# Kernel optimization log

Measured on AMD Instinct MI355X. Metric: run time of the kernel, lower is better.

The kernel has to match this reference:

```python
import jax, jax.numpy as jnp
import numpy as np

N_E = 4096
E_DIM = 512
BETA = 0.25


def setup_inputs() -> dict:
    key = jax.random.key(0)
    k1, k2 = jax.random.split(key)
    z = jax.random.normal(k1, (32, 512, E_DIM), dtype=jnp.float32)
    # embedding.weight ~ U(-1/n_e, 1/n_e)
    emb = jax.random.uniform(k2, (N_E, E_DIM), dtype=jnp.float32,
                             minval=-1.0 / N_E, maxval=1.0 / N_E)
    return {"z": z, "emb": emb}


def reference(z, emb):
    B, S, D = z.shape
    zf = z.reshape(-1, D)  # (N, D)
    # squared L2 distances: ||z||^2 + ||e||^2 - 2 z @ e^T  -> (N, n_e)
    d = (jnp.sum(zf * zf, axis=1, keepdims=True)
         + jnp.sum(emb * emb, axis=1)
         - 2.0 * jnp.matmul(zf, emb.T))
    idx = jnp.argmin(d, axis=1)  # (N,)
    z_q = emb[idx].reshape(z.shape)

    # commitment / codebook loss (detach = stop_gradient)
    loss = (jnp.mean((z_q - jax.lax.stop_gradient(z)) ** 2)
            + BETA * jnp.mean((jax.lax.stop_gradient(z_q) - z) ** 2))

    # straight-through estimator
    z_q_st = z + jax.lax.stop_gradient(z_q - z)

    # perplexity via codeword usage histogram (equiv. to mean of one-hots)
    N = zf.shape[0]
    counts = jnp.zeros((N_E,), dtype=z.dtype).at[idx].add(1.0)
    e_mean = counts / N
    perplexity = jnp.exp(-jnp.sum(e_mean * jnp.log(e_mean + 1e-10)))

    return (loss, z_q_st, idx, perplexity)
```

## Files before the change

### kernel.cpp

```cpp
#include <hip/hip_runtime.h>
#include <math.h>

#define NROWS 16384
#define DDIM  512
#define NE    4096
#define NZ    (NROWS * DDIM)
#define MAXC  64
#define MARGIN 2e-3f

typedef __attribute__((ext_vector_type(8))) short bf16x8;
typedef __attribute__((ext_vector_type(4))) float f32x4;

__device__ __forceinline__ float sqr_rn(float x) { return __fmul_rn(x, x); }
__device__ __forceinline__ ushort f2bf(float f) {
    const unsigned u = __float_as_uint(f);
    return (ushort)((u + 0x7fffu + ((u >> 16) & 1u)) >> 16);
}
__device__ __forceinline__ unsigned pack2(float a, float b) {
    return (unsigned)f2bf(a) | ((unsigned)f2bf(b) << 16);
}

__global__ void k_prep(const float* __restrict__ z, const float* __restrict__ emb,
                       ushort* __restrict__ zh, ushort* __restrict__ eh,
                       float* __restrict__ znorm, float* __restrict__ bnorm,
                       unsigned* __restrict__ counts) {
    if (blockIdx.x < 1024) {
        const int lane = threadIdx.x & 63;
        const int c = (int)((blockIdx.x * 256 + threadIdx.x) >> 6);
        const float4* p = (const float4*)(emb + (size_t)c * DDIM);
        const float4 v0 = p[lane * 2], v1 = p[lane * 2 + 1];
        uint4 w; w.x = pack2(v0.x, v0.y); w.y = pack2(v0.z, v0.w);
        w.z = pack2(v1.x, v1.y); w.w = pack2(v1.z, v1.w);
        *(uint4*)(eh + (size_t)c * DDIM + lane * 8) = w;
        float s = v0.x*v0.x + v0.y*v0.y + v0.z*v0.z + v0.w*v0.w
                + v1.x*v1.x + v1.y*v1.y + v1.z*v1.z + v1.w*v1.w;
        #pragma unroll
        for (int m = 32; m; m >>= 1) s += __shfl_xor(s, m);
        if (lane == 0) { bnorm[c] = s; counts[c] = 0u; }
    } else {
        const int t = (int)((blockIdx.x - 1024) * 256 + threadIdx.x);
        const int row = t >> 2, blk = t & 3;
        const float4* p = (const float4*)(z + (size_t)row * DDIM + blk * 128);
        ushort* zo = zh + (size_t)row * DDIM + blk * 128;
        float4 v0 = p[0], v1 = p[1];
        {
            uint4 w; w.x = pack2(v0.x, v0.y); w.y = pack2(v0.z, v0.w);
            w.z = pack2(v1.x, v1.y); w.w = pack2(v1.z, v1.w);
            *(uint4*)zo = w;
        }
        float r[8];
        r[0] = sqr_rn(v0.x); r[1] = sqr_rn(v0.y); r[2] = sqr_rn(v0.z); r[3] = sqr_rn(v0.w);
        r[4] = sqr_rn(v1.x); r[5] = sqr_rn(v1.y); r[6] = sqr_rn(v1.z); r[7] = sqr_rn(v1.w);
        #pragma unroll
        for (int i = 1; i < 16; ++i) {
            v0 = p[2 * i]; v1 = p[2 * i + 1];
            uint4 w; w.x = pack2(v0.x, v0.y); w.y = pack2(v0.z, v0.w);
            w.z = pack2(v1.x, v1.y); w.w = pack2(v1.z, v1.w);
            *(uint4*)(zo + i * 8) = w;
            r[0] = __fadd_rn(r[0], sqr_rn(v0.x)); r[1] = __fadd_rn(r[1], sqr_rn(v0.y));
            r[2] = __fadd_rn(r[2], sqr_rn(v0.z)); r[3] = __fadd_rn(r[3], sqr_rn(v0.w));
            r[4] = __fadd_rn(r[4], sqr_rn(v1.x)); r[5] = __fadd_rn(r[5], sqr_rn(v1.y));
            r[6] = __fadd_rn(r[6], sqr_rn(v1.z)); r[7] = __fadd_rn(r[7], sqr_rn(v1.w));
        }
        const float B = __fadd_rn(__fadd_rn(__fadd_rn(r[0], r[1]), __fadd_rn(r[2], r[3])),
                                  __fadd_rn(__fadd_rn(r[4], r[5]), __fadd_rn(r[6], r[7])));
        const float s01 = __fadd_rn(B, __shfl_xor(B, 1));
        const float zn  = __fadd_rn(s01, __shfl_xor(s01, 2));
        if (blk == 0) znorm[row] = zn;
    }
}

__global__ __launch_bounds__(256) void k_mfma(const ushort* __restrict__ zh,
                                              const ushort* __restrict__ eh,
                                              const float* __restrict__ bnorm,
                                              ushort* __restrict__ sbuf,
                                              float* __restrict__ rowblkmin) {
    __shared__ ushort Af[2][8 * 512];
    __shared__ ushort Bf[2][8 * 512];
    const int tid = threadIdx.x;
    const int lane = tid & 63;
    const int w = tid >> 6;
    const int wrow = (w >> 1) * 64, wcol = (w & 1) * 64;
    const int rbase = blockIdx.x * 128, cbase = blockIdx.y * 128;
    const int sr = tid >> 1, sh = tid & 1;
    const int g  = sr >> 4, r15 = sr & 15;
    const int r16 = lane & 15, g4 = (lane >> 4) * 4;
    const int soff = g * 512 + r15 * 8 + sh * 4;

    const ushort* ga = zh + (size_t)(rbase + sr) * DDIM + sh * 16;
    const ushort* gb = eh + (size_t)(cbase + sr) * DDIM + sh * 16;

    f32x4 acc[4][4];
    #pragma unroll
    for (int i = 0; i < 4; ++i)
        #pragma unroll
        for (int j = 0; j < 4; ++j) acc[i][j] = (f32x4){0.f, 0.f, 0.f, 0.f};

    {
        const uint4 qa0 = *(const uint4*)ga;
        const uint4 qa1 = *(const uint4*)(ga + 8);
        const uint4 qb0 = *(const uint4*)gb;
        const uint4 qb1 = *(const uint4*)(gb + 8);
        ushort* pa = &Af[0][soff];
        *(uint2*)(pa +   0) = make_uint2(qa0.x, qa0.y);
        *(uint2*)(pa + 128) = make_uint2(qa0.z, qa0.w);
        *(uint2*)(pa + 256) = make_uint2(qa1.x, qa1.y);
        *(uint2*)(pa + 384) = make_uint2(qa1.z, qa1.w);
        ushort* pb = &Bf[0][soff];
        *(uint2*)(pb +   0) = make_uint2(qb0.x, qb0.y);
        *(uint2*)(pb + 128) = make_uint2(qb0.z, qb0.w);
        *(uint2*)(pb + 256) = make_uint2(qb1.x, qb1.y);
        *(uint2*)(pb + 384) = make_uint2(qb1.z, qb1.w);
    }
    __syncthreads();

    for (int kb = 0; kb < DDIM; kb += 32) {
        const int cur = (kb >> 5) & 1;
        const bool more = (kb + 32 < DDIM);
        uint4 na0, na1, nb0, nb1;
        if (more) {
            na0 = *(const uint4*)(ga + kb + 32);
            na1 = *(const uint4*)(ga + kb + 40);
            nb0 = *(const uint4*)(gb + kb + 32);
            nb1 = *(const uint4*)(gb + kb + 40);
        }
        bf16x8 af[4], bf[4];
        #pragma unroll
        for (int f = 0; f < 4; ++f) {
            af[f] = *(const bf16x8*)&Af[cur][((wrow >> 4) + f) * 512 + lane * 8];
            bf[f] = *(const bf16x8*)&Bf[cur][((wcol >> 4) + f) * 512 + lane * 8];
        }
        #pragma unroll
        for (int fi = 0; fi < 4; ++fi)
            #pragma unroll
            for (int fj = 0; fj < 4; ++fj)
                acc[fi][fj] = __builtin_amdgcn_mfma_f32_16x16x32_bf16(
                    af[fi], bf[fj], acc[fi][fj], 0, 0, 0);
        if (more) {
            ushort* pa = &Af[cur ^ 1][soff];
            *(uint2*)(pa +   0) = make_uint2(na0.x, na0.y);
            *(uint2*)(pa + 128) = make_uint2(na0.z, na0.w);
            *(uint2*)(pa + 256) = make_uint2(na1.x, na1.y);
            *(uint2*)(pa + 384) = make_uint2(na1.z, na1.w);
            ushort* pb = &Bf[cur ^ 1][soff];
            *(uint2*)(pb +   0) = make_uint2(nb0.x, nb0.y);
            *(uint2*)(pb + 128) = make_uint2(nb0.z, nb0.w);
            *(uint2*)(pb + 256) = make_uint2(nb1.x, nb1.y);
            *(uint2*)(pb + 384) = make_uint2(nb1.z, nb1.w);
            __syncthreads();
        }
    }

    float bn[4];
    #pragma unroll
    for (int fj = 0; fj < 4; ++fj) bn[fj] = bnorm[cbase + wcol + fj * 16 + r16];

    #pragma unroll
    for (int fi = 0; fi < 4; ++fi) {
        #pragma unroll
        for (int r = 0; r < 4; ++r) {
            const int row = rbase + wrow + fi * 16 + g4 + r;
            float s[4];
            #pragma unroll
            for (int fj = 0; fj < 4; ++fj) s[fj] = fmaf(-2.f, acc[fi][fj][r], bn[fj]);
            uint2* sp = (uint2*)(sbuf + (size_t)row * NE + cbase + wcol);
            sp[r16] = make_uint2(pack2(s[0], s[1]), pack2(s[2], s[3]));
            float m = fminf(fminf(s[0], s[1]), fminf(s[2], s[3]));
            #pragma unroll
            for (int x = 1; x < 16; x <<= 1) m = fminf(m, __shfl_xor(m, x));
            if (r16 == 0)
                rowblkmin[(size_t)row * 64 + blockIdx.y * 2 + (w & 1)] = m;
        }
    }
}

__device__ __forceinline__ unsigned long long exact_key(const float4* __restrict__ zp4,
                                                        const float* __restrict__ emb,
                                                        const float* __restrict__ bnorm,
                                                        float zn, int c) {
    const float4* ep4 = (const float4*)(emb + (size_t)c * DDIM);
    float acc = 0.f;
    #pragma unroll 8
    for (int q = 0; q < DDIM / 4; ++q) {
        const float4 zv = zp4[q];
        const float4 ev = ep4[q];
        acc = fmaf(zv.x, ev.x, acc);
        acc = fmaf(zv.y, ev.y, acc);
        acc = fmaf(zv.z, ev.z, acc);
        acc = fmaf(zv.w, ev.w, acc);
    }
    const float s = __fsub_rn(__fadd_rn(zn, bnorm[c]), __fmul_rn(2.f, acc));
    return ((unsigned long long)__float_as_uint(s) << 32) | (unsigned)c;
}

__global__ void k_pg(const ushort* __restrict__ sbuf, const float* __restrict__ rowblkmin,
                     const float* __restrict__ z, const float* __restrict__ emb,
                     const float* __restrict__ znorm, const float* __restrict__ bnorm,
                     float* __restrict__ out, unsigned* __restrict__ counts,
                     float* __restrict__ d2buf) {
    __shared__ int candL[4][MAXC];
    __shared__ unsigned cntL[4];
    const int lane = threadIdx.x & 63;
    const int w = threadIdx.x >> 6;
    const int row = blockIdx.x * 4 + w;
    if (threadIdx.x < 4) cntL[threadIdx.x] = 0u;
    __syncthreads();

    const float bm = rowblkmin[(size_t)row * 64 + lane];
    float gmin = bm;
    #pragma unroll
    for (int m = 32; m; m >>= 1) gmin = fminf(gmin, __shfl_xor(gmin, m));
    const float thr = gmin + MARGIN;
    unsigned long long bmask = __ballot(bm <= thr);
    while (bmask) {
        const int b = __builtin_ctzll(bmask); bmask &= bmask - 1;
        const float val = __uint_as_float(
            (unsigned)sbuf[(size_t)row * NE + b * 64 + lane] << 16);
        if (val <= thr) {
            const unsigned slot = atomicAdd(&cntL[w], 1u);
            if (slot < MAXC)
                candL[w][slot] = b * 64 + (lane & 3) * 16 + (lane >> 2);
        }
    }
    __syncthreads();

    const int cnt = (int)cntL[w];
    int id;
    if (cnt == 1) {
        id = candL[w][0] & (NE - 1);
    } else {
        const float zn = znorm[row];
        const float4* zp4 = (const float4*)(z + (size_t)row * DDIM);
        unsigned long long best = ~0ULL;
        if (cnt >= 2 && cnt <= MAXC) {
            if (lane < cnt)
                best = exact_key(zp4, emb, bnorm, zn, candL[w][lane] & (NE - 1));
        } else {
            for (int c = lane; c < NE; c += 64) {
                const unsigned long long k = exact_key(zp4, emb, bnorm, zn, c);
                if (k < best) best = k;
            }
        }
        #pragma unroll
        for (int m = 32; m; m >>= 1) {
            const unsigned long long ov = __shfl_xor(best, m);
            if (ov < best) best = ov;
        }
        id = (int)(__shfl(best, 0) & (unsigned long long)(NE - 1));
    }

    const float* zp = z + (size_t)row * DDIM;
    const float* ep = emb + (size_t)id * DDIM;
    float* op = out + 1 + (size_t)row * DDIM;
    float d2 = 0.f;
    #pragma unroll
    for (int m = 0; m < 8; ++m) {
        const int k = m * 64 + lane;
        const float e = ep[k];
        const float zv = zp[k];
        const float t = e - zv;
        op[k] = zv + t;
        d2 = fmaf(t, t, d2);
    }
    #pragma unroll
    for (int m = 32; m; m >>= 1) d2 += __shfl_xor(d2, m);
    if (lane == 0) {
        atomicAdd(&counts[id], 1u);
        d2buf[row] = d2;
        out[1 + (size_t)NZ + row] = (float)id;
    }
}

__global__ void k_final(const float* __restrict__ d2buf, const unsigned* __restrict__ counts,
                        float* __restrict__ out) {
    __shared__ double sh[256];
    __shared__ float  shf[256];
    const int tid = threadIdx.x;
    double ent = 0.0;
    for (int i = tid; i < NE; i += 256) {
        const double p = (double)counts[i] / (double)NROWS;
        ent += p * log(p + 1e-10);
    }
    float sse = 0.f;
    for (int i = tid; i < NROWS; i += 256) sse += d2buf[i];
    sh[tid] = ent; shf[tid] = sse;
    __syncthreads();
    for (int s = 128; s; s >>= 1) {
        if (tid < s) { sh[tid] += sh[tid + s]; shf[tid] += shf[tid + s]; }
        __syncthreads();
    }
    if (tid == 0) {
        out[0] = 1.25f * (shf[0] / (float)NZ);
        out[1 + (size_t)NZ + NROWS] = (float)exp(-sh[0]);
    }
}

extern "C" void kernel_launch(void* const* d_in, const int* in_sizes, int n_in,
                              void* d_out, int out_size, void* d_ws, size_t ws_size,
                              hipStream_t stream) {
    const float* z   = (const float*)d_in[0];
    const float* emb = (const float*)d_in[1];
    float* out = (float*)d_out;
    char* ws = (char*)d_ws;

    ushort* zh = (ushort*)(out + 4);
    ushort* eh = (ushort*)(out + 4 + 4194304);

    size_t off = 0;
    float*    bnorm  = (float*)(ws + off); off += (size_t)NE * 4;
    unsigned* counts = (unsigned*)(ws + off); off += (size_t)NE * 4;
    float*    d2buf  = (float*)(ws + off); off += (size_t)NROWS * 4;
    float*    znorm  = (float*)(ws + off); off += (size_t)NROWS * 4;
    ushort*   sbuf   = (ushort*)(ws + off); off += (size_t)NROWS * NE * 2;
    float*    rowblkmin = (float*)(ws + off); off += (size_t)NROWS * 64 * 4;

    k_prep<<<1280, 256, 0, stream>>>(z, emb, zh, eh, znorm, bnorm, counts);
    k_mfma<<<dim3(NROWS / 128, NE / 128), 256, 0, stream>>>(zh, eh, bnorm, sbuf, rowblkmin);
    k_pg<<<NROWS / 4, 256, 0, stream>>>(sbuf, rowblkmin, z, emb, znorm, bnorm, out, counts, d2buf);
    k_final<<<1, 256, 0, stream>>>(d2buf, counts, out);
}
```

Measured before the change: 275.0 us.

## Replace full bf16 score buffer with per-block top-2 candidate summaries

The matmul kernel no longer writes the full 16384x4096 bf16 distance matrix. For each row and 64-column block it keeps the two smallest order-preserving keys plus a count of near-minimum entries, and the selection kernel builds its candidate list from these summaries. The aim is to remove a 128 MB global write and the scattered rereads. Crowded blocks (more than two near-ties) now fall back to exact checks on all 64 columns, or to a full scan of the row. This adds shuffle work to the matmul epilogue.

```diff
diff --git a/kernel.cpp b/kernel.cpp
--- a/kernel.cpp
+++ b/kernel.cpp
@@ -5,7 +5,7 @@
 #define DDIM  512
 #define NE    4096
 #define NZ    (NROWS * DDIM)
-#define MAXC  64
+#define MAXC  128
 #define MARGIN 2e-3f
 
 typedef __attribute__((ext_vector_type(8))) short bf16x8;
@@ -18,6 +18,16 @@
 }
 __device__ __forceinline__ unsigned pack2(float a, float b) {
     return (unsigned)f2bf(a) | ((unsigned)f2bf(b) << 16);
+}
+__device__ __forceinline__ unsigned ordkey(float s, int col) {
+    const ushort b = f2bf(s);
+    const ushort key16 = (b & 0x8000) ? (ushort)~b : (ushort)(b | 0x8000);
+    return ((unsigned)key16 << 16) | (unsigned)col;
+}
+__device__ __forceinline__ float dec_key(unsigned p) {
+    const ushort key16 = (ushort)(p >> 16);
+    const ushort b = (key16 & 0x8000) ? (ushort)(key16 & 0x7fff) : (ushort)~key16;
+    return __uint_as_float((unsigned)b << 16);
 }
 
 __global__ void k_prep(const float* __restrict__ z, const float* __restrict__ emb,
@@ -73,7 +83,7 @@
 __global__ __launch_bounds__(256) void k_mfma(const ushort* __restrict__ zh,
                                               const ushort* __restrict__ eh,
                                               const float* __restrict__ bnorm,
-                                              ushort* __restrict__ sbuf,
+                                              unsigned long long* __restrict__ cand2,
                                               float* __restrict__ rowblkmin) {
     __shared__ ushort Af[2][8 * 512];
     __shared__ ushort Bf[2][8 * 512];
@@ -154,6 +164,7 @@
     float bn[4];
     #pragma unroll
     for (int fj = 0; fj < 4; ++fj) bn[fj] = bnorm[cbase + wcol + fj * 16 + r16];
+    const unsigned long long gmask = 0xFFFFULL << ((lane >> 4) * 16);
 
     #pragma unroll
     for (int fi = 0; fi < 4; ++fi) {
@@ -163,13 +174,34 @@
             float s[4];
             #pragma unroll
             for (int fj = 0; fj < 4; ++fj) s[fj] = fmaf(-2.f, acc[fi][fj][r], bn[fj]);
-            uint2* sp = (uint2*)(sbuf + (size_t)row * NE + cbase + wcol);
-            sp[r16] = make_uint2(pack2(s[0], s[1]), pack2(s[2], s[3]));
             float m = fminf(fminf(s[0], s[1]), fminf(s[2], s[3]));
             #pragma unroll
             for (int x = 1; x < 16; x <<= 1) m = fminf(m, __shfl_xor(m, x));
-            if (r16 == 0)
-                rowblkmin[(size_t)row * 64 + blockIdx.y * 2 + (w & 1)] = m;
+            const float thrB = m + MARGIN;
+            int cnt = 0;
+            unsigned k[4];
+            #pragma unroll
+            for (int fj = 0; fj < 4; ++fj) {
+                cnt += __popcll(__ballot(s[fj] <= thrB) & gmask);
+                k[fj] = ordkey(s[fj], cbase + wcol + fj * 16 + r16);
+            }
+            unsigned a0 = min(k[0], k[1]), a1 = max(k[0], k[1]);
+            unsigned b0 = min(k[2], k[3]), b1 = max(k[2], k[3]);
+            unsigned m1 = min(a0, b0);
+            unsigned m2 = min(max(a0, b0), min(a1, b1));
+            #pragma unroll
+            for (int x = 1; x < 16; x <<= 1) {
+                const unsigned o1 = __shfl_xor(m1, x), o2 = __shfl_xor(m2, x);
+                const unsigned n1 = min(m1, o1);
+                m2 = min(max(m1, o1), min(m2, o2));
+                m1 = n1;
+            }
+            if (r16 == 0) {
+                const int slot = (int)blockIdx.y * 2 + (w & 1);
+                rowblkmin[(size_t)row * 64 + slot] = m;
+                m2 = (m2 & 0xFFFF0FFFu) | ((unsigned)min(cnt, 15) << 12);
+                cand2[(size_t)row * 64 + slot] = ((unsigned long long)m1 << 32) | m2;
+            }
         }
     }
 }
@@ -193,18 +225,16 @@
     return ((unsigned long long)__float_as_uint(s) << 32) | (unsigned)c;
 }
 
-__global__ void k_pg(const ushort* __restrict__ sbuf, const float* __restrict__ rowblkmin,
+__global__ void k_pg(const unsigned long long* __restrict__ cand2,
+                     const float* __restrict__ rowblkmin,
                      const float* __restrict__ z, const float* __restrict__ emb,
                      const float* __restrict__ znorm, const float* __restrict__ bnorm,
                      float* __restrict__ out, unsigned* __restrict__ counts,
                      float* __restrict__ d2buf) {
     __shared__ int candL[4][MAXC];
-    __shared__ unsigned cntL[4];
     const int lane = threadIdx.x & 63;
     const int w = threadIdx.x >> 6;
     const int row = blockIdx.x * 4 + w;
-    if (threadIdx.x < 4) cntL[threadIdx.x] = 0u;
-    __syncthreads();
 
     const float bm = rowblkmin[(size_t)row * 64 + lane];
     float gmin = bm;
@@ -212,33 +242,44 @@
     for (int m = 32; m; m >>= 1) gmin = fminf(gmin, __shfl_xor(gmin, m));
     const float thr = gmin + MARGIN;
     unsigned long long bmask = __ballot(bm <= thr);
+    int kc = 0;
+    bool fullscan = false;
     while (bmask) {
         const int b = __builtin_ctzll(bmask); bmask &= bmask - 1;
-        const float val = __uint_as_float(
-            (unsigned)sbuf[(size_t)row * NE + b * 64 + lane] << 16);
-        if (val <= thr) {
-            const unsigned slot = atomicAdd(&cntL[w], 1u);
-            if (slot < MAXC)
-                candL[w][slot] = b * 64 + (lane & 3) * 16 + (lane >> 2);
-        }
-    }
-    __syncthreads();
-
-    const int cnt = (int)cntL[w];
+        const unsigned long long cd = cand2[(size_t)row * 64 + b];
+        const unsigned p1 = (unsigned)(cd >> 32), p2 = (unsigned)cd;
+        const int cnt = (int)((p2 >> 12) & 0xFu);
+        if (cnt > 2) {
+            if (kc + 64 <= MAXC) candL[w][kc + lane] = b * 64 + lane;
+            else fullscan = true;
+            kc += 64;
+        } else {
+            if (dec_key(p1) <= thr) {
+                if (lane == 0 && kc < MAXC) candL[w][kc] = (int)(p1 & 0xFFFu);
+                ++kc;
+            }
+            if (dec_key(p2) <= thr) {
+                if (lane == 0 && kc < MAXC) candL[w][kc] = (int)(p2 & 0xFFFu);
+                ++kc;
+            }
+        }
+    }
+    if (kc > MAXC) fullscan = true;
+
     int id;
-    if (cnt == 1) {
+    if (!fullscan && kc == 1) {
         id = candL[w][0] & (NE - 1);
     } else {
         const float zn = znorm[row];
         const float4* zp4 = (const float4*)(z + (size_t)row * DDIM);
         unsigned long long best = ~0ULL;
-        if (cnt >= 2 && cnt <= MAXC) {
-            if (lane < cnt)
-                best = exact_key(zp4, emb, bnorm, zn, candL[w][lane] & (NE - 1));
+        if (!fullscan) {
+            for (int i = lane; i < kc; i += 64)
+                best = min(best, exact_key(zp4, emb, bnorm, zn, candL[w][i] & (NE - 1)));
         } else {
             for (int c = lane; c < NE; c += 64) {
-                const unsigned long long k = exact_key(zp4, emb, bnorm, zn, c);
-                if (k < best) best = k;
+                const unsigned long long kk = exact_key(zp4, emb, bnorm, zn, c);
+                if (kk < best) best = kk;
             }
         }
         #pragma unroll
@@ -311,11 +352,12 @@
     unsigned* counts = (unsigned*)(ws + off); off += (size_t)NE * 4;
     float*    d2buf  = (float*)(ws + off); off += (size_t)NROWS * 4;
     float*    znorm  = (float*)(ws + off); off += (size_t)NROWS * 4;
-    ushort*   sbuf   = (ushort*)(ws + off); off += (size_t)NROWS * NE * 2;
     float*    rowblkmin = (float*)(ws + off); off += (size_t)NROWS * 64 * 4;
+    unsigned long long* cand2 = (unsigned long long*)(ws + off);
+    off += (size_t)NROWS * 64 * 8;
 
     k_prep<<<1280, 256, 0, stream>>>(z, emb, zh, eh, znorm, bnorm, counts);
-    k_mfma<<<dim3(NROWS / 128, NE / 128), 256, 0, stream>>>(zh, eh, bnorm, sbuf, rowblkmin);
-    k_pg<<<NROWS / 4, 256, 0, stream>>>(sbuf, rowblkmin, z, emb, znorm, bnorm, out, counts, d2buf);
+    k_mfma<<<dim3(NROWS / 128, NE / 128), 256, 0, stream>>>(zh, eh, bnorm, cand2, rowblkmin);
+    k_pg<<<NROWS / 4, 256, 0, stream>>>(cand2, rowblkmin, z, emb, znorm, bnorm, out, counts, d2buf);
     k_final<<<1, 256, 0, stream>>>(d2buf, counts, out);
 }
```

Result: slower. 864.1 us (+214.2%).
